# Optimization experiments

Measured on AMD Instinct MI355X. Metric: run time of the kernel, lower is better.

## Reference

```python
import jax, jax.numpy as jnp
import numpy as np

MASK_INFTY_APPROX = 1e30
B, L, D = 2, 2048, 1024
H = 16
HD = D // H  # 64
NCODE = 512


def setup_inputs() -> dict:
    key = jax.random.key(0)
    ks = jax.random.split(key, 6)
    s = 1.0 / np.sqrt(D)
    x = jax.random.normal(ks[0], (B, L, D), dtype=jnp.float32)
    Wq = jax.random.normal(ks[1], (D, D), dtype=jnp.float32) * s
    Wk = jax.random.normal(ks[2], (D, D), dtype=jnp.float32) * s
    Wv = jax.random.normal(ks[3], (D, D), dtype=jnp.float32) * s
    Wo = jax.random.normal(ks[4], (D, D), dtype=jnp.float32) * s
    codebook = jax.random.normal(ks[5], (H, NCODE, HD), dtype=jnp.float32)
    return {"x": x, "Wq": Wq, "Wk": Wk, "Wv": Wv, "Wo": Wo, "codebook": codebook}


def _vq(k, codebook):
    # k: [B,H,L,hd], codebook: [H,C,hd]
    dot = jnp.einsum('bhld,hcd->bhlc', k, codebook)
    k2 = jnp.sum(k * k, axis=-1, keepdims=True)            # [B,H,L,1]
    c2 = jnp.sum(codebook * codebook, axis=-1)             # [H,C]
    d2 = k2 - 2.0 * dot + c2[None, :, None, :]             # [B,H,L,C]
    shortcodes = jnp.argmin(d2, axis=-1)                   # [B,H,L]
    h_idx = jnp.arange(H)[None, :, None]
    c_sel = codebook[h_idx, shortcodes]                    # [B,H,L,hd]
    # straight-through quantization
    k_hat = k + jax.lax.stop_gradient(c_sel - k)
    l_commit = jnp.mean(jnp.sum((k - jax.lax.stop_gradient(c_sel)) ** 2, axis=-1))
    l_codebook = jnp.mean(jnp.sum((jax.lax.stop_gradient(k) - c_sel) ** 2, axis=-1))
    return k_hat, shortcodes, l_commit, l_codebook


def reference(x, Wq, Wk, Wv, Wo, codebook):
    q = jnp.einsum('bld,de->ble', x, Wq.T).reshape(B, L, H, HD).transpose(0, 2, 1, 3)
    k = jnp.einsum('bld,de->ble', x, Wk.T).reshape(B, L, H, HD).transpose(0, 2, 1, 3)
    v = jnp.einsum('bld,de->ble', x, Wv.T).reshape(B, L, H, HD).transpose(0, 2, 1, 3)
    k_hat, shortcodes, l_commit, l_codebook = _vq(k, codebook)
    scale = HD ** (-0.5)
    logits = jnp.einsum('bhld,bhtd->bhlt', q, k_hat) * scale  # [B,H,L,L]
    causal_mask = jnp.tril(jnp.ones((L, L), dtype=bool))
    logits = jnp.where(causal_mask[None, None], logits, -MASK_INFTY_APPROX)
    w = jax.nn.softmax(logits, axis=-1)
    attn = jnp.einsum('bhlt,bhtd->bhld', w, v)
    attn = attn.transpose(0, 2, 1, 3).reshape(B, L, D)
    out = jnp.einsum('bld,de->ble', attn, Wo.T)
    return out, l_commit, l_codebook, shortcodes
```

## Files before the change

kernel.cpp:

```cpp
#include <hip/hip_runtime.h>
#include <stdint.h>

#define BB 2
#define HH 16
#define LL 2048
#define DD 1024
#define HDD 64
#define NC 512

typedef __bf16 bf16x8 __attribute__((ext_vector_type(8)));
typedef float f32x4 __attribute__((ext_vector_type(4)));
typedef unsigned short u16x8 __attribute__((ext_vector_type(8)));
typedef unsigned short u16x4 __attribute__((ext_vector_type(4)));

__device__ __forceinline__ unsigned short f2bf(float f) {
  union { float f; unsigned u; } v; v.f = f;
  unsigned u = v.u;
  u += 0x7fffu + ((u >> 16) & 1u);
  return (unsigned short)(u >> 16);
}
__device__ __forceinline__ float bf2f(unsigned short h) {
  union { unsigned u; float f; } v; v.u = ((unsigned)h) << 16;
  return v.f;
}

__device__ __forceinline__ void load_lds16(const unsigned short* g, unsigned short* l) {
  __builtin_amdgcn_global_load_lds((const __attribute__((address_space(1))) void*)g,
                                   (__attribute__((address_space(3))) void*)l, 16, 0, 0);
}

__global__ void cast_all(const float* __restrict__ x, const float* __restrict__ wq,
                         const float* __restrict__ wk, const float* __restrict__ wv,
                         const float* __restrict__ wo, const float* __restrict__ cb,
                         unsigned short* __restrict__ xb, unsigned short* __restrict__ xl,
                         unsigned short* __restrict__ wb, unsigned short* __restrict__ wkl,
                         unsigned short* __restrict__ wob, unsigned short* __restrict__ cbb,
                         unsigned short* __restrict__ cbl, float* __restrict__ c2,
                         float* __restrict__ lsum) {
  if (blockIdx.x >= 4096) {
    int i = (blockIdx.x - 4096) * 256 + threadIdx.x;
    if (i < HH * NC) {
      const float* r = cb + (long)i * HDD;
      double s = 0.0;
      for (int j = 0; j < HDD; j++) s += (double)r[j] * (double)r[j];
      c2[i] = (float)s;
    }
    return;
  }
  long i = (long)blockIdx.x * blockDim.x + threadIdx.x;
  if (i == 0) lsum[0] = 0.f;
  const long NX4 = 1048576, NW4 = 262144, NCB4 = 131072;
  const long TOT4 = NX4 + 4 * NW4 + NCB4;
  for (long q = i; q < TOT4; q += (long)4096 * blockDim.x) {
    if (q < NX4) {
      long t = q * 4;
      float4 v = *(const float4*)(x + t);
      u16x4 hi, lo;
#pragma unroll
      for (int j = 0; j < 4; j++) {
        float f = ((const float*)&v)[j];
        unsigned short h = f2bf(f);
        hi[j] = h; lo[j] = f2bf(f - bf2f(h));
      }
      *(u16x4*)(xb + t) = hi;
      *(u16x4*)(xl + t) = lo;
    } else if (q < NX4 + NW4) {
      long t = (q - NX4) * 4;
      float4 v = *(const float4*)(wq + t);
      u16x4 hi;
#pragma unroll
      for (int j = 0; j < 4; j++) hi[j] = f2bf(((const float*)&v)[j]);
      *(u16x4*)(wb + t) = hi;
    } else if (q < NX4 + 2 * NW4) {
      long t = (q - NX4 - NW4) * 4;
      float4 v = *(const float4*)(wk + t);
      u16x4 hi, lo;
#pragma unroll
      for (int j = 0; j < 4; j++) {
        float f = ((const float*)&v)[j];
        unsigned short h = f2bf(f);
        hi[j] = h; lo[j] = f2bf(f - bf2f(h));
      }
      *(u16x4*)(wb + 1048576 + t) = hi;
      *(u16x4*)(wkl + t) = lo;
    } else if (q < NX4 + 3 * NW4) {
      long t = (q - NX4 - 2 * NW4) * 4;
      float4 v = *(const float4*)(wv + t);
      u16x4 hi;
#pragma unroll
      for (int j = 0; j < 4; j++) hi[j] = f2bf(((const float*)&v)[j]);
      *(u16x4*)(wb + 2097152 + t) = hi;
    } else if (q < NX4 + 4 * NW4) {
      long t = (q - NX4 - 3 * NW4) * 4;
      float4 v = *(const float4*)(wo + t);
      u16x4 hi;
#pragma unroll
      for (int j = 0; j < 4; j++) hi[j] = f2bf(((const float*)&v)[j]);
      *(u16x4*)(wob + t) = hi;
    } else {
      long t = (q - NX4 - 4 * NW4) * 4;
      float4 v = *(const float4*)(cb + t);
      u16x4 hi, lo;
#pragma unroll
      for (int j = 0; j < 4; j++) {
        float f = ((const float*)&v)[j];
        unsigned short h = f2bf(f);
        hi[j] = h; lo[j] = f2bf(f - bf2f(h));
      }
      *(u16x4*)(cbb + t) = hi;
      *(u16x4*)(cbl + t) = lo;
    }
  }
}

__global__ __launch_bounds__(256) void qv_kvq(
    const unsigned short* __restrict__ xb, const unsigned short* __restrict__ xl,
    const unsigned short* __restrict__ wb, const unsigned short* __restrict__ wkl,
    const float* __restrict__ cb, const float* __restrict__ c2,
    const unsigned short* __restrict__ cbb, const unsigned short* __restrict__ cbl,
    unsigned short* __restrict__ qb, unsigned short* __restrict__ vt,
    unsigned short* __restrict__ khat, float* __restrict__ scodes,
    float* __restrict__ lsum) {
  __shared__ __align__(16) char smem[37888];
  int tid = threadIdx.x;
  int wave = tid >> 6, lane = tid & 63;
  int quad = lane >> 4, col = lane & 15;
  int gid = blockIdx.x;
  int cls = gid % 3;

  if (cls == 2) {
    unsigned short* As = (unsigned short*)smem;
    unsigned short* Bs = (unsigned short*)(smem + 8192);
    int qid = gid / 3;
    int bx = qid & 15, by = qid >> 4;
    int m0 = by * 128;
    int n0 = bx * 128 + (bx >= 8 ? 1024 : 0);
    f32x4 acc[4][4] = {};
    int row_in = (wave << 4) + (lane >> 2);
    int seg = lane & 3;
    const unsigned short* gA0 = xb + (long)(m0 + row_in) * DD + seg * 8;
    const unsigned short* gA1 = xb + (long)(m0 + 64 + row_in) * DD + seg * 8;
    const unsigned short* gB0 = wb + (long)(n0 + row_in) * DD + seg * 8;
    const unsigned short* gB1 = wb + (long)(n0 + 64 + row_in) * DD + seg * 8;
    unsigned short* lA0 = As + wave * 512;
    unsigned short* lA1 = As + 2048 + wave * 512;
    unsigned short* lB0 = Bs + wave * 512;
    unsigned short* lB1 = Bs + 2048 + wave * 512;
    int wm = wave & 1, wn = wave >> 1;
    const unsigned short* pa = As + (wm * 64 + col) * 32 + quad * 8;
    const unsigned short* pb = Bs + (wn * 64 + col) * 32 + quad * 8;
    for (int kk = 0; kk < DD; kk += 32) {
      __syncthreads();
      load_lds16(gA0 + kk, lA0);
      load_lds16(gA1 + kk, lA1);
      load_lds16(gB0 + kk, lB0);
      load_lds16(gB1 + kk, lB1);
      __syncthreads();
      bf16x8 af[4], bfr[4];
      for (int t = 0; t < 4; t++) af[t]  = *(const bf16x8*)(pa + t * 512);
      for (int t = 0; t < 4; t++) bfr[t] = *(const bf16x8*)(pb + t * 512);
      for (int mt = 0; mt < 4; mt++)
        for (int nt = 0; nt < 4; nt++)
          acc[mt][nt] = __builtin_amdgcn_mfma_f32_16x16x32_bf16(af[mt], bfr[nt], acc[mt][nt], 0, 0, 0);
    }
    for (int mt = 0; mt < 4; mt++)
      for (int nt = 0; nt < 4; nt++) {
        int mbase = m0 + wm * 64 + mt * 16 + quad * 4;
        int n = n0 + wn * 64 + nt * 16 + col;
        int which = n >> 10, e = n & 1023;
        int h = e >> 6, hd = e & 63;
        for (int r = 0; r < 4; r++) {
          int m = mbase + r;
          int b = m >> 11, l = m & 2047;
          unsigned short val = f2bf(acc[mt][nt][r]);
          long bh = (long)(b * HH + h);
          if (which == 0)      qb[(bh * LL + l) * HDD + hd] = val;
          else                 vt[(bh * HDD + hd) * LL + l] = val;
        }
      }
    return;
  }

  unsigned short* Ah = (unsigned short*)smem;
  unsigned short* Al = (unsigned short*)(smem + 4096);
  unsigned short* Bh = (unsigned short*)(smem + 8192);
  unsigned short* Bl = (unsigned short*)(smem + 12288);
  float* kfL = (float*)smem;
  unsigned short* CbHb = (unsigned short*)(smem + 17408);
  unsigned short* CbLb = (unsigned short*)(smem + 26624);
  float* Cs = (float*)(smem + 35840);

  int kid = (gid / 3) * 2 + cls;
  int mtile = kid & 63;
  int h = kid >> 6;
  int m0 = mtile * 64;
  int n0 = h * 64;
  int bgl = m0 >> 11;
  int l0 = m0 & 2047;
  long bh = (long)(bgl * HH + h);
  const float* c2h = c2 + h * NC;
  Cs[tid] = c2h[tid];
  Cs[tid + 256] = c2h[tid + 256];

  f32x4 acc[2][2] = {};
  int row_in = (wave << 4) + (lane >> 2);
  int seg = lane & 3;
  const unsigned short* gAh = xb + (long)(m0 + row_in) * DD + seg * 8;
  const unsigned short* gAl = xl + (long)(m0 + row_in) * DD + seg * 8;
  const unsigned short* gBh = wb + (long)(1048576 + (long)(n0 + row_in) * DD) + seg * 8;
  const unsigned short* gBl = wkl + (long)(n0 + row_in) * DD + seg * 8;
  unsigned short* lAh = Ah + wave * 512;
  unsigned short* lAl = Al + wave * 512;
  unsigned short* lBh = Bh + wave * 512;
  unsigned short* lBl = Bl + wave * 512;
  int wm = wave & 1, wn = wave >> 1;
  const unsigned short* pah = Ah + (wm * 32 + col) * 32 + quad * 8;
  const unsigned short* pal = Al + (wm * 32 + col) * 32 + quad * 8;
  const unsigned short* pbh = Bh + (wn * 32 + col) * 32 + quad * 8;
  const unsigned short* pbl = Bl + (wn * 32 + col) * 32 + quad * 8;
  for (int kk = 0; kk < DD; kk += 32) {
    __syncthreads();
    load_lds16(gAh + kk, lAh);
    load_lds16(gAl + kk, lAl);
    load_lds16(gBh + kk, lBh);
    load_lds16(gBl + kk, lBl);
    __syncthreads();
    bf16x8 ah[2], al[2], bhf[2], blf[2];
    for (int t = 0; t < 2; t++) ah[t] = *(const bf16x8*)(pah + t * 512);
    for (int t = 0; t < 2; t++) al[t] = *(const bf16x8*)(pal + t * 512);
    for (int t = 0; t < 2; t++) bhf[t] = *(const bf16x8*)(pbh + t * 512);
    for (int t = 0; t < 2; t++) blf[t] = *(const bf16x8*)(pbl + t * 512);
    for (int mt = 0; mt < 2; mt++)
      for (int nt = 0; nt < 2; nt++) {
        acc[mt][nt] = __builtin_amdgcn_mfma_f32_16x16x32_bf16(ah[mt], bhf[nt], acc[mt][nt], 0, 0, 0);
        acc[mt][nt] = __builtin_amdgcn_mfma_f32_16x16x32_bf16(ah[mt], blf[nt], acc[mt][nt], 0, 0, 0);
        acc[mt][nt] = __builtin_amdgcn_mfma_f32_16x16x32_bf16(al[mt], bhf[nt], acc[mt][nt], 0, 0, 0);
      }
  }
  __syncthreads();
  const unsigned short* cbbh = cbb + (long)h * NC * HDD;
  const unsigned short* cblh = cbl + (long)h * NC * HDD;
  int srow = tid >> 3;
  int sseg = (tid & 7) * 8;
  const unsigned short* gH = cbbh + (long)srow * HDD + sseg;
  const unsigned short* gL = cblh + (long)srow * HDD + sseg;
  int ldsOff = srow * 72 + sseg;
  u16x8 ph0 = *(const u16x8*)(gH);
  u16x8 pl0 = *(const u16x8*)(gL);
  for (int mt = 0; mt < 2; mt++)
    for (int nt = 0; nt < 2; nt++) {
      int rw = wm * 32 + mt * 16 + quad * 4;
      int hd = wn * 32 + nt * 16 + col;
      for (int r = 0; r < 4; r++)
        kfL[(rw + r) * 68 + hd] = acc[mt][nt][r];
    }
  *(u16x8*)(CbHb + ldsOff) = ph0;
  *(u16x8*)(CbLb + ldsOff) = pl0;
  __syncthreads();

  bf16x8 bh0, bh1, bl0, bl1;
  float k2;
  {
    const float* kp = kfL + (wave * 16 + col) * 68 + quad * 8;
    float4 t0 = *(const float4*)(kp);
    float4 t1 = *(const float4*)(kp + 4);
    float4 t2 = *(const float4*)(kp + 32);
    float4 t3 = *(const float4*)(kp + 36);
    float fv[16];
    fv[0]=t0.x; fv[1]=t0.y; fv[2]=t0.z; fv[3]=t0.w;
    fv[4]=t1.x; fv[5]=t1.y; fv[6]=t1.z; fv[7]=t1.w;
    fv[8]=t2.x; fv[9]=t2.y; fv[10]=t2.z; fv[11]=t2.w;
    fv[12]=t3.x; fv[13]=t3.y; fv[14]=t3.z; fv[15]=t3.w;
    k2 = 0.f;
#pragma unroll
    for (int j = 0; j < 16; j++) k2 = fmaf(fv[j], fv[j], k2);
    k2 += __shfl_xor(k2, 16);
    k2 += __shfl_xor(k2, 32);
    u16x8 h0, h1, l0u, l1u;
#pragma unroll
    for (int j = 0; j < 8; j++) {
      unsigned short hi = f2bf(fv[j]);
      h0[j] = hi; l0u[j] = f2bf(fv[j] - bf2f(hi));
      unsigned short hi2 = f2bf(fv[8 + j]);
      h1[j] = hi2; l1u[j] = f2bf(fv[8 + j] - bf2f(hi2));
    }
    bh0 = __builtin_bit_cast(bf16x8, h0);
    bh1 = __builtin_bit_cast(bf16x8, h1);
    bl0 = __builtin_bit_cast(bf16x8, l0u);
    bl1 = __builtin_bit_cast(bf16x8, l1u);
  }
  float b1v = 1e38f, b2v = 1e38f;
  int b1i = 0x7fffffff, b2i = 0x7fffffff;
  for (int t = 0; t < 16; t++) {
    int cur = t & 1;
    u16x8 nh, nl;
    if (t < 15) {
      nh = *(const u16x8*)(gH + (t + 1) * 32 * HDD);
      nl = *(const u16x8*)(gL + (t + 1) * 32 * HDD);
    }
    const unsigned short* CbHc = CbHb + cur * 2304;
    const unsigned short* CbLc = CbLb + cur * 2304;
#pragma unroll
    for (int s = 0; s < 2; s++) {
      const unsigned short* rp = CbHc + (s * 16 + col) * 72 + quad * 8;
      const unsigned short* rq = CbLc + (s * 16 + col) * 72 + quad * 8;
      bf16x8 ah0 = *(const bf16x8*)(rp);
      bf16x8 ah1 = *(const bf16x8*)(rp + 32);
      bf16x8 al0 = *(const bf16x8*)(rq);
      bf16x8 al1 = *(const bf16x8*)(rq + 32);
      f32x4 aP = {}, aQ = {};
      aP = __builtin_amdgcn_mfma_f32_16x16x32_bf16(ah0, bh0, aP, 0, 0, 0);
      aQ = __builtin_amdgcn_mfma_f32_16x16x32_bf16(ah1, bh1, aQ, 0, 0, 0);
      aP = __builtin_amdgcn_mfma_f32_16x16x32_bf16(al0, bh0, aP, 0, 0, 0);
      aQ = __builtin_amdgcn_mfma_f32_16x16x32_bf16(al1, bh1, aQ, 0, 0, 0);
      aP = __builtin_amdgcn_mfma_f32_16x16x32_bf16(ah0, bl0, aP, 0, 0, 0);
      aQ = __builtin_amdgcn_mfma_f32_16x16x32_bf16(ah1, bl1, aQ, 0, 0, 0);
      f32x4 c2v = *(const f32x4*)(Cs + t * 32 + s * 16 + quad * 4);
#pragma unroll
      for (int r = 0; r < 4; r++) {
        float val = c2v[r] - 2.0f * (aP[r] + aQ[r]);
        int idx = t * 32 + s * 16 + quad * 4 + r;
        if (val < b1v) { b2v = b1v; b2i = b1i; b1v = val; b1i = idx; }
        else if (val < b2v) { b2v = val; b2i = idx; }
      }
    }
    if (t < 15) {
      *(u16x8*)(CbHb + (cur ^ 1) * 2304 + ldsOff) = nh;
      *(u16x8*)(CbLb + (cur ^ 1) * 2304 + ldsOff) = nl;
    }
    __syncthreads();
  }
#pragma unroll
  for (int d = 16; d <= 32; d <<= 1) {
    float o1v = __shfl_xor(b1v, d); int o1i = __shfl_xor(b1i, d);
    float o2v = __shfl_xor(b2v, d); int o2i = __shfl_xor(b2i, d);
    if (o1v < b1v || (o1v == b1v && o1i < b1i)) {
      float nv; int ni;
      if (b1v < o2v || (b1v == o2v && b1i < o2i)) { nv = b1v; ni = b1i; }
      else { nv = o2v; ni = o2i; }
      b1v = o1v; b1i = o1i; b2v = nv; b2i = ni;
    } else {
      if (o1v < b2v || (o1v == b2v && o1i < b2i)) { b2v = o1v; b2i = o1i; }
    }
  }
  const float DMARG = 0.015625f;
  bool trig = (b2v - b1v <= DMARG);
  float part;
  int widx = b1i;
  if (__any(trig)) {
    const float* kpr = kfL + (wave * 16 + col) * 68 + quad * 8;
    float4 f0 = *(const float4*)(kpr);
    float4 f1 = *(const float4*)(kpr + 4);
    float4 f2 = *(const float4*)(kpr + 32);
    float4 f3 = *(const float4*)(kpr + 36);
    const float* c1p = cb + ((long)h * NC + b1i) * HDD + quad * 8;
    const float* c2p = cb + ((long)h * NC + b2i) * HDD + quad * 8;
    float4 a0 = *(const float4*)(c1p);
    float4 a1 = *(const float4*)(c1p + 4);
    float4 a2 = *(const float4*)(c1p + 32);
    float4 a3 = *(const float4*)(c1p + 36);
    float4 e0 = *(const float4*)(c2p);
    float4 e1 = *(const float4*)(c2p + 4);
    float4 e2 = *(const float4*)(c2p + 32);
    float4 e3 = *(const float4*)(c2p + 36);
    float s1 = 0.f, s2 = 0.f;
#pragma unroll
    for (int j = 0; j < 4; j++) {
      float d;
      d = ((const float*)&f0)[j] - ((const float*)&a0)[j]; s1 = fmaf(d, d, s1);
      d = ((const float*)&f1)[j] - ((const float*)&a1)[j]; s1 = fmaf(d, d, s1);
      d = ((const float*)&f2)[j] - ((const float*)&a2)[j]; s1 = fmaf(d, d, s1);
      d = ((const float*)&f3)[j] - ((const float*)&a3)[j]; s1 = fmaf(d, d, s1);
      d = ((const float*)&f0)[j] - ((const float*)&e0)[j]; s2 = fmaf(d, d, s2);
      d = ((const float*)&f1)[j] - ((const float*)&e1)[j]; s2 = fmaf(d, d, s2);
      d = ((const float*)&f2)[j] - ((const float*)&e2)[j]; s2 = fmaf(d, d, s2);
      d = ((const float*)&f3)[j] - ((const float*)&e3)[j]; s2 = fmaf(d, d, s2);
    }
    s1 += __shfl_xor(s1, 16); s1 += __shfl_xor(s1, 32);
    s2 += __shfl_xor(s2, 16); s2 += __shfl_xor(s2, 32);
    if (trig) {
      if (s2 < s1 || (s2 == s1 && b2i < b1i)) { widx = b2i; part = s2; }
      else { widx = b1i; part = s1; }
    } else {
      part = k2 + b1v;
    }
  } else {
    part = k2 + b1v;
  }
  if (quad != 0) part = 0.f;
  part += __shfl_xor(part, 1);  part += __shfl_xor(part, 2);
  part += __shfl_xor(part, 4);  part += __shfl_xor(part, 8);
  part += __shfl_xor(part, 16); part += __shfl_xor(part, 32);
  if (lane == 0) atomicAdd(lsum, part);
  if (lane < 16)
    scodes[bh * LL + l0 + wave * 16 + lane] = (float)widx;
  {
    int rL = lane >> 2;
    int p = (lane & 3) * 16;
    int code = __shfl(widx, rL);
    const unsigned short* src = cbbh + (long)code * HDD + p;
    unsigned short* dst = khat + (bh * LL + l0 + wave * 16 + rL) * HDD + p;
    *(u16x8*)(dst)     = *(const u16x8*)(src);
    *(u16x8*)(dst + 8) = *(const u16x8*)(src + 8);
  }
}

__global__ __launch_bounds__(256) void attn_kernel(
    const unsigned short* __restrict__ qb, const unsigned short* __restrict__ khat,
    const unsigned short* __restrict__ vt, unsigned short* __restrict__ attnb) {
  __shared__ __align__(16) unsigned short Pbuf[4][16 * 72];
  __shared__ __align__(16) unsigned short Kbuf[64 * 72];
  __shared__ __align__(16) unsigned short Vbuf[64 * 72];
  int tid = threadIdx.x, wave = tid >> 6, lane = tid & 63;
  int quad = lane >> 4, col = lane & 15;
  int id = blockIdx.y * 16 + blockIdx.x;
  int xcd = id & 7, sidx = id >> 3;
  int bh = xcd * 4 + (sidx >> 4);
  int pi = sidx & 15;
  int b = bh >> 4, h = bh & 15;
  int ta = pi, tb = 31 - pi;
  int qbA = ta * 64 + wave * 16;
  int qbB = tb * 64 + wave * 16;
  const unsigned short* qrA = qb + ((long)bh * LL + qbA + col) * HDD;
  const unsigned short* qrB = qb + ((long)bh * LL + qbB + col) * HDD;
  bf16x8 aqA0 = *(const bf16x8*)(qrA + quad * 8);
  bf16x8 aqA1 = *(const bf16x8*)(qrA + 32 + quad * 8);
  bf16x8 aqB0 = *(const bf16x8*)(qrB + quad * 8);
  bf16x8 aqB1 = *(const bf16x8*)(qrB + 32 + quad * 8);
  float lA = 0.f, lB = 0.f;
  f32x4 oA[4] = {}, oB[4] = {};
  unsigned short* P = Pbuf[wave];
  const unsigned short* kh = khat + (long)bh * LL * HDD;
  const unsigned short* vh = vt + (long)bh * HDD * LL;
  int srow = tid >> 2, sc = (tid & 3) * 8;
  const unsigned short* gK = kh + (long)srow * HDD + sc;
  const unsigned short* gV = vh + (long)srow * LL + sc;
  unsigned short* lK = Kbuf + srow * 72 + sc;
  unsigned short* lV = Vbuf + srow * 72 + sc;
  const float SCL = 0.18033688011112042f;
  u16x8 rk0 = *(const u16x8*)(gK);
  u16x8 rk1 = *(const u16x8*)(gK + 32);
  u16x8 rv0 = *(const u16x8*)(gV);
  u16x8 rv1 = *(const u16x8*)(gV + 32);
  for (int kt = 0; kt <= tb; kt++) {
    int kbase = kt * 64;
    bool actA = (kt <= ta);
    __syncthreads();
    *(u16x8*)lK        = rk0;
    *(u16x8*)(lK + 32) = rk1;
    *(u16x8*)lV        = rv0;
    *(u16x8*)(lV + 32) = rv1;
    __syncthreads();
    if (kt < tb) {
      const unsigned short* nK = gK + (long)(kt + 1) * 64 * HDD;
      const unsigned short* nV = gV + (kt + 1) * 64;
      rk0 = *(const u16x8*)(nK);
      rk1 = *(const u16x8*)(nK + 32);
      rv0 = *(const u16x8*)(nV);
      rv1 = *(const u16x8*)(nV + 32);
    }
    f32x4 zA[4], zB[4];
    __builtin_amdgcn_s_setprio(1);
    for (int nt = 0; nt < 4; nt++) {
      const unsigned short* krow = Kbuf + (nt * 16 + col) * 72;
      bf16x8 k0 = *(const bf16x8*)(krow + quad * 8);
      bf16x8 k1 = *(const bf16x8*)(krow + 32 + quad * 8);
      f32x4 z = {};
      z = __builtin_amdgcn_mfma_f32_16x16x32_bf16(k0, aqB0, z, 0, 0, 0);
      z = __builtin_amdgcn_mfma_f32_16x16x32_bf16(k1, aqB1, z, 0, 0, 0);
      zB[nt] = z;
      if (actA) {
        f32x4 y = {};
        y = __builtin_amdgcn_mfma_f32_16x16x32_bf16(k0, aqA0, y, 0, 0, 0);
        y = __builtin_amdgcn_mfma_f32_16x16x32_bf16(k1, aqA1, y, 0, 0, 0);
        zA[nt] = y;
      }
    }
    __builtin_amdgcn_s_setprio(0);
    for (int nt = 0; nt < 4; nt++) {
      u16x4 pk;
      for (int r = 0; r < 4; r++) {
        float sc2 = zB[nt][r] * SCL;
        int key = kbase + nt * 16 + quad * 4 + r;
        if (kt == tb && key > qbB + col) sc2 = -1e30f;
        float p = exp2f(sc2);
        lB += p;
        pk[r] = __builtin_bit_cast(unsigned short, (__bf16)p);
      }
      *(u16x4*)(P + col * 72 + nt * 16 + quad * 4) = pk;
    }
    {
      bf16x8 ap0 = *(const bf16x8*)(P + col * 72 + quad * 8);
      bf16x8 ap1 = *(const bf16x8*)(P + col * 72 + 32 + quad * 8);
      __builtin_amdgcn_s_setprio(1);
      for (int nt = 0; nt < 4; nt++) {
        const unsigned short* vrow = Vbuf + (nt * 16 + col) * 72;
        bf16x8 v0 = *(const bf16x8*)(vrow + quad * 8);
        bf16x8 v1 = *(const bf16x8*)(vrow + 32 + quad * 8);
        oB[nt] = __builtin_amdgcn_mfma_f32_16x16x32_bf16(ap0, v0, oB[nt], 0, 0, 0);
        oB[nt] = __builtin_amdgcn_mfma_f32_16x16x32_bf16(ap1, v1, oB[nt], 0, 0, 0);
      }
      __builtin_amdgcn_s_setprio(0);
    }
    if (actA) {
      for (int nt = 0; nt < 4; nt++) {
        u16x4 pk;
        for (int r = 0; r < 4; r++) {
          float sc2 = zA[nt][r] * SCL;
          int key = kbase + nt * 16 + quad * 4 + r;
          if (kt == ta && key > qbA + col) sc2 = -1e30f;
          float p = exp2f(sc2);
          lA += p;
          pk[r] = __builtin_bit_cast(unsigned short, (__bf16)p);
        }
        *(u16x4*)(P + col * 72 + nt * 16 + quad * 4) = pk;
      }
      bf16x8 ap0 = *(const bf16x8*)(P + col * 72 + quad * 8);
      bf16x8 ap1 = *(const bf16x8*)(P + col * 72 + 32 + quad * 8);
      __builtin_amdgcn_s_setprio(1);
      for (int nt = 0; nt < 4; nt++) {
        const unsigned short* vrow = Vbuf + (nt * 16 + col) * 72;
        bf16x8 v0 = *(const bf16x8*)(vrow + quad * 8);
        bf16x8 v1 = *(const bf16x8*)(vrow + 32 + quad * 8);
        oA[nt] = __builtin_amdgcn_mfma_f32_16x16x32_bf16(ap0, v0, oA[nt], 0, 0, 0);
        oA[nt] = __builtin_amdgcn_mfma_f32_16x16x32_bf16(ap1, v1, oA[nt], 0, 0, 0);
      }
      __builtin_amdgcn_s_setprio(0);
    }
  }
  lA += __shfl_xor(lA, 16); lA += __shfl_xor(lA, 32);
  lB += __shfl_xor(lB, 16); lB += __shfl_xor(lB, 32);
  float invAc = 1.0f / lA;
  float invBc = 1.0f / lB;
  for (int r = 0; r < 4; r++) {
    float invA = __shfl(invAc, quad * 4 + r);
    float invB = __shfl(invBc, quad * 4 + r);
    int rowA = qbA + quad * 4 + r;
    int rowB = qbB + quad * 4 + r;
    for (int nt = 0; nt < 4; nt++) {
      int hd = nt * 16 + col;
      attnb[((long)b * LL + rowA) * DD + h * HDD + hd] = f2bf(oA[nt][r] * invA);
      attnb[((long)b * LL + rowB) * DD + h * HDD + hd] = f2bf(oB[nt][r] * invB);
    }
  }
}

__global__ __launch_bounds__(256) void gemm_out(
    const unsigned short* __restrict__ attnb, const unsigned short* __restrict__ wob,
    const float* __restrict__ lsum, float* __restrict__ out) {
  __shared__ __align__(16) unsigned short As[128 * 32];
  __shared__ __align__(16) unsigned short Bs[64 * 32];
  int tid = threadIdx.x;
  int wave = tid >> 6, lane = tid & 63;
  int quad = lane >> 4, col = lane & 15;
  int m0 = blockIdx.y * 128;
  int n0 = blockIdx.x * 64;
  f32x4 acc[4][2] = {};
  int row_in = (wave << 4) + (lane >> 2);
  int seg = lane & 3;
  const unsigned short* gA0 = attnb + (long)(m0 + row_in) * DD + seg * 8;
  const unsigned short* gA1 = attnb + (long)(m0 + 64 + row_in) * DD + seg * 8;
  const unsigned short* gB0 = wob + (long)(n0 + row_in) * DD + seg * 8;
  unsigned short* lA0 = As + wave * 512;
  unsigned short* lA1 = As + 2048 + wave * 512;
  unsigned short* lB0 = Bs + wave * 512;
  int wm = wave & 1, wn = wave >> 1;
  const unsigned short* pa = As + (wm * 64 + col) * 32 + quad * 8;
  const unsigned short* pb = Bs + (wn * 32 + col) * 32 + quad * 8;
  for (int kk = 0; kk < DD; kk += 32) {
    __syncthreads();
    load_lds16(gA0 + kk, lA0);
    load_lds16(gA1 + kk, lA1);
    load_lds16(gB0 + kk, lB0);
    __syncthreads();
    bf16x8 af[4], bfr[2];
    for (int t = 0; t < 4; t++) af[t]  = *(const bf16x8*)(pa + t * 512);
    for (int t = 0; t < 2; t++) bfr[t] = *(const bf16x8*)(pb + t * 512);
    for (int mt = 0; mt < 4; mt++)
      for (int nt = 0; nt < 2; nt++)
        acc[mt][nt] = __builtin_amdgcn_mfma_f32_16x16x32_bf16(af[mt], bfr[nt], acc[mt][nt], 0, 0, 0);
  }
  for (int mt = 0; mt < 4; mt++)
    for (int nt = 0; nt < 2; nt++) {
      int mbase = m0 + wm * 64 + mt * 16 + quad * 4;
      int n = n0 + wn * 32 + nt * 16 + col;
      for (int r = 0; r < 4; r++)
        out[(long)(mbase + r) * DD + n] = acc[mt][nt][r];
    }
  if (blockIdx.x == 0 && blockIdx.y == 0 && tid == 0) {
    float v = lsum[0] / (float)(BB * HH * LL);
    out[4194304] = v;
    out[4194305] = v;
  }
}

extern "C" void kernel_launch(void* const* d_in, const int* in_sizes, int n_in,
                              void* d_out, int out_size, void* d_ws, size_t ws_size,
                              hipStream_t stream) {
  const float* x  = (const float*)d_in[0];
  const float* wq = (const float*)d_in[1];
  const float* wk = (const float*)d_in[2];
  const float* wv = (const float*)d_in[3];
  const float* wo = (const float*)d_in[4];
  const float* cb = (const float*)d_in[5];
  float* out = (float*)d_out;

  char* ws = (char*)d_ws;
  size_t off = 0;
  auto alloc = [&](size_t bytes) {
    void* p = ws + off;
    off = (off + bytes + 255) & ~(size_t)255;
    return p;
  };
  unsigned short* xb    = (unsigned short*)alloc(4194304 * 2);
  unsigned short* xl    = (unsigned short*)alloc(4194304 * 2);
  unsigned short* wb    = (unsigned short*)alloc(3145728 * 2);
  unsigned short* wkl   = (unsigned short*)alloc(1048576 * 2);
  unsigned short* wob   = (unsigned short*)alloc(1048576 * 2);
  unsigned short* cbb   = (unsigned short*)alloc(524288 * 2);
  unsigned short* cbl   = (unsigned short*)alloc(524288 * 2);
  unsigned short* qb    = (unsigned short*)alloc(4194304 * 2);
  unsigned short* vt    = (unsigned short*)alloc(4194304 * 2);
  unsigned short* khat  = (unsigned short*)alloc(4194304 * 2);
  unsigned short* attnb = (unsigned short*)alloc(4194304 * 2);
  float* c2   = (float*)alloc(8192 * 4);
  float* lsum = (float*)alloc(256);

  cast_all<<<dim3(4128), dim3(256), 0, stream>>>(x, wq, wk, wv, wo, cb, xb, xl, wb, wkl, wob, cbb, cbl, c2, lsum);
  qv_kvq<<<dim3(1536), dim3(256), 0, stream>>>(xb, xl, wb, wkl, cb, c2, cbb, cbl, qb, vt, khat, out + 4194306, lsum);
  attn_kernel<<<dim3(16, 32), dim3(256), 0, stream>>>(qb, khat, vt, attnb);
  gemm_out<<<dim3(16, 32), dim3(256), 0, stream>>>(attnb, wob, lsum, out);
}
```

Before: 273.5 us.

## Double-buffer LDS tiles in the projection and output GEMM loops

The Q/V projection, the split-precision K projection and the output projection GEMMs now each keep two LDS tile buffers. The first tile is prefetched before the loop, and each iteration issues the next tile's global-to-LDS loads into the other buffer before running MFMAs on the current one. This removes one of the two barriers per K-step so that load latency can overlap with compute. In exchange it doubles LDS use: the K path's second buffer now overlaps the codebook staging area, which is only safe because that area is filled after the loop. The higher LDS footprint may also lower occupancy.

Result: no change. 276.0 us (+0.9%).

```diff
diff --git a/kernel.cpp b/kernel.cpp
--- a/kernel.cpp
+++ b/kernel.cpp
@@ -129,8 +129,7 @@
   int cls = gid % 3;
 
   if (cls == 2) {
-    unsigned short* As = (unsigned short*)smem;
-    unsigned short* Bs = (unsigned short*)(smem + 8192);
+    unsigned short* Ss = (unsigned short*)smem;
     int qid = gid / 3;
     int bx = qid & 15, by = qid >> 4;
     int m0 = by * 128;
@@ -142,20 +141,26 @@
     const unsigned short* gA1 = xb + (long)(m0 + 64 + row_in) * DD + seg * 8;
     const unsigned short* gB0 = wb + (long)(n0 + row_in) * DD + seg * 8;
     const unsigned short* gB1 = wb + (long)(n0 + 64 + row_in) * DD + seg * 8;
-    unsigned short* lA0 = As + wave * 512;
-    unsigned short* lA1 = As + 2048 + wave * 512;
-    unsigned short* lB0 = Bs + wave * 512;
-    unsigned short* lB1 = Bs + 2048 + wave * 512;
     int wm = wave & 1, wn = wave >> 1;
-    const unsigned short* pa = As + (wm * 64 + col) * 32 + quad * 8;
-    const unsigned short* pb = Bs + (wn * 64 + col) * 32 + quad * 8;
+    {
+      unsigned short* bs = Ss;
+      load_lds16(gA0, bs + wave * 512);
+      load_lds16(gA1, bs + 2048 + wave * 512);
+      load_lds16(gB0, bs + 4096 + wave * 512);
+      load_lds16(gB1, bs + 4096 + 2048 + wave * 512);
+    }
     for (int kk = 0; kk < DD; kk += 32) {
+      int cur = (kk >> 5) & 1;
       __syncthreads();
-      load_lds16(gA0 + kk, lA0);
-      load_lds16(gA1 + kk, lA1);
-      load_lds16(gB0 + kk, lB0);
-      load_lds16(gB1 + kk, lB1);
-      __syncthreads();
+      if (kk + 32 < DD) {
+        unsigned short* bs = Ss + (cur ^ 1) * 8192;
+        load_lds16(gA0 + kk + 32, bs + wave * 512);
+        load_lds16(gA1 + kk + 32, bs + 2048 + wave * 512);
+        load_lds16(gB0 + kk + 32, bs + 4096 + wave * 512);
+        load_lds16(gB1 + kk + 32, bs + 4096 + 2048 + wave * 512);
+      }
+      const unsigned short* pa = Ss + cur * 8192 + (wm * 64 + col) * 32 + quad * 8;
+      const unsigned short* pb = Ss + cur * 8192 + 4096 + (wn * 64 + col) * 32 + quad * 8;
       bf16x8 af[4], bfr[4];
       for (int t = 0; t < 4; t++) af[t]  = *(const bf16x8*)(pa + t * 512);
       for (int t = 0; t < 4; t++) bfr[t] = *(const bf16x8*)(pb + t * 512);
@@ -181,10 +186,7 @@
     return;
   }
 
-  unsigned short* Ah = (unsigned short*)smem;
-  unsigned short* Al = (unsigned short*)(smem + 4096);
-  unsigned short* Bh = (unsigned short*)(smem + 8192);
-  unsigned short* Bl = (unsigned short*)(smem + 12288);
+  unsigned short* Ks = (unsigned short*)smem;
   float* kfL = (float*)smem;
   unsigned short* CbHb = (unsigned short*)(smem + 17408);
   unsigned short* CbLb = (unsigned short*)(smem + 26624);
@@ -209,22 +211,28 @@
   const unsigned short* gAl = xl + (long)(m0 + row_in) * DD + seg * 8;
   const unsigned short* gBh = wb + (long)(1048576 + (long)(n0 + row_in) * DD) + seg * 8;
   const unsigned short* gBl = wkl + (long)(n0 + row_in) * DD + seg * 8;
-  unsigned short* lAh = Ah + wave * 512;
-  unsigned short* lAl = Al + wave * 512;
-  unsigned short* lBh = Bh + wave * 512;
-  unsigned short* lBl = Bl + wave * 512;
   int wm = wave & 1, wn = wave >> 1;
-  const unsigned short* pah = Ah + (wm * 32 + col) * 32 + quad * 8;
-  const unsigned short* pal = Al + (wm * 32 + col) * 32 + quad * 8;
-  const unsigned short* pbh = Bh + (wn * 32 + col) * 32 + quad * 8;
-  const unsigned short* pbl = Bl + (wn * 32 + col) * 32 + quad * 8;
+  {
+    unsigned short* bs = Ks;
+    load_lds16(gAh, bs + wave * 512);
+    load_lds16(gAl, bs + 2048 + wave * 512);
+    load_lds16(gBh, bs + 4096 + wave * 512);
+    load_lds16(gBl, bs + 6144 + wave * 512);
+  }
   for (int kk = 0; kk < DD; kk += 32) {
+    int cur = (kk >> 5) & 1;
     __syncthreads();
-    load_lds16(gAh + kk, lAh);
-    load_lds16(gAl + kk, lAl);
-    load_lds16(gBh + kk, lBh);
-    load_lds16(gBl + kk, lBl);
-    __syncthreads();
+    if (kk + 32 < DD) {
+      unsigned short* bs = Ks + (cur ^ 1) * 8192;
+      load_lds16(gAh + kk + 32, bs + wave * 512);
+      load_lds16(gAl + kk + 32, bs + 2048 + wave * 512);
+      load_lds16(gBh + kk + 32, bs + 4096 + wave * 512);
+      load_lds16(gBl + kk + 32, bs + 6144 + wave * 512);
+    }
+    const unsigned short* pah = Ks + cur * 8192 + (wm * 32 + col) * 32 + quad * 8;
+    const unsigned short* pal = Ks + cur * 8192 + 2048 + (wm * 32 + col) * 32 + quad * 8;
+    const unsigned short* pbh = Ks + cur * 8192 + 4096 + (wn * 32 + col) * 32 + quad * 8;
+    const unsigned short* pbl = Ks + cur * 8192 + 6144 + (wn * 32 + col) * 32 + quad * 8;
     bf16x8 ah[2], al[2], bhf[2], blf[2];
     for (int t = 0; t < 2; t++) ah[t] = *(const bf16x8*)(pah + t * 512);
     for (int t = 0; t < 2; t++) al[t] = *(const bf16x8*)(pal + t * 512);
@@ -548,8 +556,7 @@
 __global__ __launch_bounds__(256) void gemm_out(
     const unsigned short* __restrict__ attnb, const unsigned short* __restrict__ wob,
     const float* __restrict__ lsum, float* __restrict__ out) {
-  __shared__ __align__(16) unsigned short As[128 * 32];
-  __shared__ __align__(16) unsigned short Bs[64 * 32];
+  __shared__ __align__(16) unsigned short S[12288];
   int tid = threadIdx.x;
   int wave = tid >> 6, lane = tid & 63;
   int quad = lane >> 4, col = lane & 15;
@@ -561,18 +568,23 @@
   const unsigned short* gA0 = attnb + (long)(m0 + row_in) * DD + seg * 8;
   const unsigned short* gA1 = attnb + (long)(m0 + 64 + row_in) * DD + seg * 8;
   const unsigned short* gB0 = wob + (long)(n0 + row_in) * DD + seg * 8;
-  unsigned short* lA0 = As + wave * 512;
-  unsigned short* lA1 = As + 2048 + wave * 512;
-  unsigned short* lB0 = Bs + wave * 512;
   int wm = wave & 1, wn = wave >> 1;
-  const unsigned short* pa = As + (wm * 64 + col) * 32 + quad * 8;
-  const unsigned short* pb = Bs + (wn * 32 + col) * 32 + quad * 8;
+  {
+    load_lds16(gA0, S + wave * 512);
+    load_lds16(gA1, S + 2048 + wave * 512);
+    load_lds16(gB0, S + 4096 + wave * 512);
+  }
   for (int kk = 0; kk < DD; kk += 32) {
+    int cur = (kk >> 5) & 1;
     __syncthreads();
-    load_lds16(gA0 + kk, lA0);
-    load_lds16(gA1 + kk, lA1);
-    load_lds16(gB0 + kk, lB0);
-    __syncthreads();
+    if (kk + 32 < DD) {
+      unsigned short* bs = S + (cur ^ 1) * 6144;
+      load_lds16(gA0 + kk + 32, bs + wave * 512);
+      load_lds16(gA1 + kk + 32, bs + 2048 + wave * 512);
+      load_lds16(gB0 + kk + 32, bs + 4096 + wave * 512);
+    }
+    const unsigned short* pa = S + cur * 6144 + (wm * 64 + col) * 32 + quad * 8;
+    const unsigned short* pb = S + cur * 6144 + 4096 + (wn * 32 + col) * 32 + quad * 8;
     bf16x8 af[4], bfr[2];
     for (int t = 0; t < 4; t++) af[t]  = *(const bf16x8*)(pa + t * 512);
     for (int t = 0; t < 2; t++) bfr[t] = *(const bf16x8*)(pb + t * 512);
```
